# Kernel optimization log

Measured on AMD Instinct MI355X. Metric: run time of the kernel, lower is better.

## Reference

```python
import jax, jax.numpy as jnp
import numpy as np

B, C = 32768, 1000
EPS = 1e-6

def setup_inputs() -> dict:
    key = jax.random.key(0)
    k1, k2 = jax.random.split(key)
    # p_tar / p_vlm are probability distributions over C classes
    p_tar = jax.nn.softmax(jax.random.normal(k1, (B, C), dtype=jnp.float32), axis=1)
    p_vlm = jax.nn.softmax(jax.random.normal(k2, (B, C), dtype=jnp.float32), axis=1)
    alpha = jnp.array([0.99], dtype=jnp.float32)  # EMA momentum
    memory_bank = jnp.full((C, C), 1.0 / C, dtype=jnp.float32)  # __init__ state
    return {"p_tar": p_tar, "p_vlm": p_vlm, "alpha": alpha, "memory_bank": memory_bank}

def _uncertainty(p):
    return -p * jnp.log(p + EPS)

def reference(p_tar, p_vlm, alpha, memory_bank):
    n_classes = memory_bank.shape[0]
    norm = 1.0 / jnp.sqrt(jnp.float32(n_classes))
    # --- class_prototype_atten (uses PRE-update memory bank, as in torch) ---
    atten = jax.nn.softmax(jnp.matmul(p_tar, memory_bank.T) * norm, axis=1)  # [B, C]
    p_tar_new = jnp.matmul(atten, memory_bank)  # [B, C]
    # --- update_membank: vectorized per-class masked-mean EMA ---
    y_tar = jnp.argmax(p_tar, axis=1)
    y_vlm = jnp.argmax(p_vlm, axis=1)
    agree = y_tar == y_vlm
    # non-agreeing rows dumped into extra segment n_classes
    seg = jnp.where(agree, y_tar, n_classes)
    sums = jax.ops.segment_sum(p_tar, seg, num_segments=n_classes + 1)[:n_classes]  # [C, C]
    counts = jax.ops.segment_sum(agree.astype(p_tar.dtype), seg, num_segments=n_classes + 1)[:n_classes]  # [C]
    has = counts > 0
    mean = sums / jnp.where(has, counts, 1.0)[:, None]
    a = alpha.reshape(())
    bank_new = jnp.where(has[:, None], a * memory_bank + (1.0 - a) * mean, memory_bank)
    # --- uncertainty_mixing ---
    eu_tar = jnp.exp(-_uncertainty(p_tar_new))
    eu_vlm = jnp.exp(-_uncertainty(p_vlm))
    p_mix = (eu_tar * p_tar_new + eu_vlm * p_vlm) / (eu_tar + eu_vlm)
    return p_mix, bank_new
```

## Files before the change

### kernel.cpp

```cpp
#include <hip/hip_runtime.h>
#include <hip/hip_bf16.h>
#include <cstdint>
#include <cstddef>

#define NROWS 32768
#define NCLS  1000
#define KP    1024
#define NCH   32

typedef unsigned short u16;
typedef __bf16 bf16x8 __attribute__((ext_vector_type(8)));
typedef float  f32x4  __attribute__((ext_vector_type(4)));


__device__ __forceinline__ void gld_lds16(const u16* g, u16* l) {
  __builtin_amdgcn_global_load_lds(
      (const __attribute__((address_space(1))) unsigned int*)g,
      (__attribute__((address_space(3))) unsigned int*)l, 16, 0, 0);
}

__global__ __launch_bounds__(128)
void prep4_bank(const float* __restrict__ bank,
                __hip_bfloat16* __restrict__ M4,
                __hip_bfloat16* __restrict__ MT4) {
  __shared__ float tile[32][33];
  const int tx = blockIdx.x;
  const int ty = blockIdx.y;
  const int t  = threadIdx.x;
  {
    const int r = t >> 2, c0 = (t & 3) * 8;
    const int gj = ty * 32 + r;
    #pragma unroll
    for (int j = 0; j < 8; ++j) {
      const int gk = tx * 32 + c0 + j;
      tile[r][c0 + j] = (gj < NCLS && gk < NCLS) ? bank[gj * NCLS + gk] : 0.0f;
    }
  }
  __syncthreads();
  const int w = t >> 6, lane = t & 63, lr = lane & 15, qq = lane >> 4;
  if (w == 0) {
    #pragma unroll
    for (int s = 0; s < 2; ++s) {
      bf16x8 o;
      #pragma unroll
      for (int j = 0; j < 8; ++j) o[j] = (__bf16)tile[s * 16 + lr][qq * 8 + j];
      *(bf16x8*)((u16*)M4 + ((size_t)(ty * 2 + s) * NCH + tx) * 512 + lane * 8) = o;
    }
  } else {
    #pragma unroll
    for (int s = 0; s < 2; ++s) {
      bf16x8 o;
      #pragma unroll
      for (int j = 0; j < 8; ++j) o[j] = (__bf16)tile[qq * 8 + j][s * 16 + lr];
      *(bf16x8*)((u16*)MT4 + ((size_t)(tx * 2 + s) * NCH + ty) * 512 + lane * 8) = o;
    }
  }
}

__global__ __launch_bounds__(256)
void rows4_kernel(const float* __restrict__ p_tar, const float* __restrict__ p_vlm,
                  __hip_bfloat16* __restrict__ A4,
                  float* __restrict__ sums, float* __restrict__ counts) {
  const int w = threadIdx.x >> 6, lane = threadIdx.x & 63;
  const int lr = lane & 15, q = lane >> 4;
  const int panel = blockIdx.x * 4 + w;
  const int row   = panel * 16 + lr;
  const float* tr = p_tar + (size_t)row * NCLS;
  const float* vr = p_vlm + (size_t)row * NCLS;
  u16* a4 = (u16*)A4 + (size_t)panel * NCH * 512 + lane * 8;

  float bvT = -1.0f; int biT = 0;
  float bvV = -1.0f; int biV = 0;
  for (int c = 0; c < NCH; ++c) {
    const int k0 = c * 32 + q * 8;
    float v[8];
    if (k0 < NCLS) {
      float4 x = *(const float4*)(tr + k0);
      float4 y = *(const float4*)(tr + k0 + 4);
      v[0] = x.x; v[1] = x.y; v[2] = x.z; v[3] = x.w;
      v[4] = y.x; v[5] = y.y; v[6] = y.z; v[7] = y.w;
    } else {
      #pragma unroll
      for (int j = 0; j < 8; ++j) v[j] = 0.0f;
    }
    bf16x8 o;
    #pragma unroll
    for (int j = 0; j < 8; ++j) {
      o[j] = (__bf16)v[j];
      if (v[j] > bvT) { bvT = v[j]; biT = k0 + j; }
    }
    *(bf16x8*)(a4 + (size_t)c * 512) = o;
    if (k0 < NCLS) {
      float4 x = *(const float4*)(vr + k0);
      float4 y = *(const float4*)(vr + k0 + 4);
      float u[8] = {x.x, x.y, x.z, x.w, y.x, y.y, y.z, y.w};
      #pragma unroll
      for (int j = 0; j < 8; ++j)
        if (u[j] > bvV) { bvV = u[j]; biV = k0 + j; }
    }
  }
  #pragma unroll
  for (int d = 16; d < 64; d <<= 1) {
    float ov = __shfl_xor(bvT, d); int oi = __shfl_xor(biT, d);
    if (ov > bvT || (ov == bvT && oi < biT)) { bvT = ov; biT = oi; }
    float ov2 = __shfl_xor(bvV, d); int oi2 = __shfl_xor(biV, d);
    if (ov2 > bvV || (ov2 == bvV && oi2 < biV)) { bvV = ov2; biV = oi2; }
  }
  const int ag = (biT == biV) ? 1 : 0;
  for (int rr = 0; rr < 16; ++rr) {
    const int agr = __shfl(ag, rr);
    if (agr) {
      const int cls = __shfl(biT, rr);
      const float* trr = p_tar + (size_t)(panel * 16 + rr) * NCLS;
      for (int k = lane; k < NCLS; k += 64)
        atomicAdd(&sums[(size_t)cls * NCLS + k], trr[k]);
      if (lane == 0) atomicAdd(&counts[cls], 1.0f);
    }
  }
}

template <int WHICH>
__global__ __launch_bounds__(256, 4)
void gemm4(const u16* __restrict__ A4, const u16* __restrict__ B4,
           __hip_bfloat16* __restrict__ E4out, float* __restrict__ rowsum,
           const float* __restrict__ p_vlm, float* __restrict__ mix_out) {
  __shared__ u16 SH[4][4096];
  const int tid  = threadIdx.x;
  const int w    = tid >> 6;
  const int lane = tid & 63;
  const int lr   = lane & 15;
  const int q    = lane >> 4;
  const int L    = blockIdx.x;
  const int xcd  = L & 7;
  const int jj   = L >> 3;
  const int bm   = xcd * 32 + (jj >> 3);
  const int bn   = jj & 7;
  const int wm   = w >> 1;
  const int wn   = w & 1;

  f32x4 acc[4][4] = {};

  const u16* ga0 = A4 + ((size_t)(bm * 8 + 2 * w) * NCH) * 512 + lane * 8;
  const u16* ga1 = ga0 + (size_t)NCH * 512;
  const u16* gb0 = B4 + ((size_t)(bn * 8 + 2 * w) * NCH) * 512 + lane * 8;
  const u16* gb1 = gb0 + (size_t)NCH * 512;

  gld_lds16(ga0, &SH[0][(2 * w + 0) * 512]);
  gld_lds16(ga1, &SH[0][(2 * w + 1) * 512]);
  gld_lds16(gb0, &SH[2][(2 * w + 0) * 512]);
  gld_lds16(gb1, &SH[2][(2 * w + 1) * 512]);

  for (int i = 0; i < NCH; ++i) {
    const int cur = i & 1;
    __syncthreads();
    if (i + 1 < NCH) {
      const int nxt = cur ^ 1;
      const size_t ko = (size_t)(i + 1) * 512;
      gld_lds16(ga0 + ko, &SH[nxt][(2 * w + 0) * 512]);
      gld_lds16(ga1 + ko, &SH[nxt][(2 * w + 1) * 512]);
      gld_lds16(gb0 + ko, &SH[2 + nxt][(2 * w + 0) * 512]);
      gld_lds16(gb1 + ko, &SH[2 + nxt][(2 * w + 1) * 512]);
    }
    bf16x8 af[4], bfr[4];
    #pragma unroll
    for (int t = 0; t < 4; ++t) {
      af[t]  = *(const bf16x8*)(&SH[cur][(wm * 4 + t) * 512 + lane * 8]);
      bfr[t] = *(const bf16x8*)(&SH[2 + cur][(wn * 4 + t) * 512 + lane * 8]);
    }
    #pragma unroll
    for (int mt = 0; mt < 4; ++mt)
      #pragma unroll
      for (int nt = 0; nt < 4; ++nt)
        acc[mt][nt] = __builtin_amdgcn_mfma_f32_16x16x32_bf16(af[mt], bfr[nt], acc[mt][nt], 0, 0, 0);
  }

  const float NORM = 0.03162277660168379f;
  if (WHICH == 1) {
    __syncthreads();
    u16* ep = &SH[w][0];
    #pragma unroll
    for (int mt = 0; mt < 4; ++mt) {
      float psum[4] = {0.f, 0.f, 0.f, 0.f};
      #pragma unroll
      for (int nt = 0; nt < 4; ++nt) {
        const int gn = bn * 128 + wn * 64 + nt * 16 + lr;
        const int cc = nt >> 1;
        const int q2 = (nt & 1) * 2 + (lr >> 3);
        const int jj2 = lr & 7;
        #pragma unroll
        for (int r = 0; r < 4; ++r) {
          float e = (gn < NCLS) ? __expf(acc[mt][nt][r] * NORM) : 0.0f;
          psum[r] += e;
          __hip_bfloat16 h = __float2bfloat16(e);
          ep[(mt * 2 + cc) * 512 + (q2 * 16 + q * 4 + r) * 8 + jj2] = *(u16*)&h;
        }
      }
      #pragma unroll
      for (int r = 0; r < 4; ++r) {
        float s = psum[r];
        s += __shfl_xor(s, 1); s += __shfl_xor(s, 2);
        s += __shfl_xor(s, 4); s += __shfl_xor(s, 8);
        if (lr == 0) atomicAdd(&rowsum[bm * 128 + wm * 64 + mt * 16 + q * 4 + r], s);
      }
    }
    #pragma unroll
    for (int ch = 0; ch < 8; ++ch) {
      const int mt = ch >> 1, cc = ch & 1;
      bf16x8 v = *(const bf16x8*)(&ep[ch * 512 + lane * 8]);
      const size_t Rg = bm * 8 + wm * 4 + mt;
      const size_t cg = bn * 4 + wn * 2 + cc;
      *(bf16x8*)((u16*)E4out + (Rg * NCH + cg) * 512 + lane * 8) = v;
    }
  } else {
    #pragma unroll
    for (int mt = 0; mt < 4; ++mt) {
      #pragma unroll
      for (int r = 0; r < 4; ++r) {
        const int gm = bm * 128 + wm * 64 + mt * 16 + q * 4 + r;
        const float inv = 1.0f / rowsum[gm];
        #pragma unroll
        for (int nt = 0; nt < 4; ++nt) {
          const int gn = bn * 128 + wn * 64 + nt * 16 + lr;
          if (gn < NCLS) {
            float pt = acc[mt][nt][r] * inv;
            float pv = p_vlm[(size_t)gm * NCLS + gn];
            float et = __expf(pt * __logf(pt + 1e-6f));
            float ev = __expf(pv * __logf(pv + 1e-6f));
            mix_out[(size_t)gm * NCLS + gn] = (et * pt + ev * pv) / (et + ev);
          }
        }
      }
    }
  }
}

__global__ __launch_bounds__(256)
void bank_update(const float* __restrict__ bank, const float* __restrict__ sums,
                 const float* __restrict__ counts, const float* __restrict__ alpha,
                 float* __restrict__ out) {
  const int idx = blockIdx.x * 256 + threadIdx.x;
  if (idx >= NCLS * NCLS) return;
  const int r = idx / NCLS;
  const float cnt = counts[r];
  const float bv  = bank[idx];
  const float a   = alpha[0];
  out[idx] = (cnt > 0.0f) ? a * bv + (1.0f - a) * (sums[idx] / cnt) : bv;
}

extern "C" void kernel_launch(void* const* d_in, const int* in_sizes, int n_in,
                              void* d_out, int out_size, void* d_ws, size_t ws_size,
                              hipStream_t stream) {
  const float* p_tar = (const float*)d_in[0];
  const float* p_vlm = (const float*)d_in[1];
  const float* alpha = (const float*)d_in[2];
  const float* bank  = (const float*)d_in[3];
  float* out_mix  = (float*)d_out;
  float* out_bank = (float*)d_out + (size_t)NROWS * NCLS;

  char* w = (char*)d_ws;
  __hip_bfloat16* A4  = (__hip_bfloat16*)w; w += (size_t)NROWS * KP * 2;
  __hip_bfloat16* E4  = (__hip_bfloat16*)w; w += (size_t)NROWS * KP * 2;
  __hip_bfloat16* M4  = (__hip_bfloat16*)w; w += (size_t)KP * KP * 2;
  __hip_bfloat16* MT4 = (__hip_bfloat16*)w; w += (size_t)KP * KP * 2;
  float* sums   = (float*)w;                w += (size_t)NCLS * NCLS * 4;
  float* counts = (float*)w;                w += 1024 * 4;
  float* rs     = (float*)w;                w += (size_t)NROWS * 4;

  hipMemsetAsync(sums, 0, (size_t)NCLS * NCLS * 4 + 1024 * 4 + (size_t)NROWS * 4, stream);

  prep4_bank<<<dim3(32, 32), 128, 0, stream>>>(bank, M4, MT4);
  rows4_kernel<<<NROWS / 64, 256, 0, stream>>>(p_tar, p_vlm, A4, sums, counts);
  gemm4<1><<<2048, 256, 0, stream>>>(
      (const u16*)A4, (const u16*)M4, E4, rs, nullptr, nullptr);
  gemm4<2><<<2048, 256, 0, stream>>>(
      (const u16*)E4, (const u16*)MT4, nullptr, rs, p_vlm, out_mix);
  bank_update<<<(NCLS * NCLS + 255) / 256, 256, 0, stream>>>(bank, sums, counts, alpha, out_bank);
}
```

Before: 549.2 us.

## Triple-buffer GEMM LDS pipeline, split row-prep across waves, simplify mixing math

The GEMM main loop moves from a double-buffered LDS pipeline to a three-stage one, using explicit vmcnt waits and a raw barrier so two K-chunks are in flight. This costs more LDS and lowers the occupancy hint from 4 to 3 blocks. The row-prep kernel now has each block own one 16-row panel, with the four waves splitting the K range and merging argmax results through shared memory; this gives more blocks and shorter per-thread loops, but only one wave issues the atomics. The mixing epilogue is rewritten algebraically to use one exp of a difference instead of two exps.

```diff
diff --git a/kernel.cpp b/kernel.cpp
--- a/kernel.cpp
+++ b/kernel.cpp
@@ -61,9 +61,11 @@
 void rows4_kernel(const float* __restrict__ p_tar, const float* __restrict__ p_vlm,
                   __hip_bfloat16* __restrict__ A4,
                   float* __restrict__ sums, float* __restrict__ counts) {
+  __shared__ float sT[4][16]; __shared__ int siT[4][16];
+  __shared__ float sV[4][16]; __shared__ int siV[4][16];
   const int w = threadIdx.x >> 6, lane = threadIdx.x & 63;
   const int lr = lane & 15, q = lane >> 4;
-  const int panel = blockIdx.x * 4 + w;
+  const int panel = blockIdx.x;
   const int row   = panel * 16 + lr;
   const float* tr = p_tar + (size_t)row * NCLS;
   const float* vr = p_vlm + (size_t)row * NCLS;
@@ -71,7 +73,7 @@
 
   float bvT = -1.0f; int biT = 0;
   float bvV = -1.0f; int biV = 0;
-  for (int c = 0; c < NCH; ++c) {
+  for (int c = w * 8; c < w * 8 + 8; ++c) {
     const int k0 = c * 32 + q * 8;
     float v[8];
     if (k0 < NCLS) {
@@ -106,25 +108,36 @@
     float ov2 = __shfl_xor(bvV, d); int oi2 = __shfl_xor(biV, d);
     if (ov2 > bvV || (ov2 == bvV && oi2 < biV)) { bvV = ov2; biV = oi2; }
   }
-  const int ag = (biT == biV) ? 1 : 0;
-  for (int rr = 0; rr < 16; ++rr) {
-    const int agr = __shfl(ag, rr);
-    if (agr) {
-      const int cls = __shfl(biT, rr);
-      const float* trr = p_tar + (size_t)(panel * 16 + rr) * NCLS;
-      for (int k = lane; k < NCLS; k += 64)
-        atomicAdd(&sums[(size_t)cls * NCLS + k], trr[k]);
-      if (lane == 0) atomicAdd(&counts[cls], 1.0f);
+  if (q == 0) { sT[w][lr] = bvT; siT[w][lr] = biT; sV[w][lr] = bvV; siV[w][lr] = biV; }
+  __syncthreads();
+  float cT = sT[0][lr]; int ciT = siT[0][lr];
+  float cV = sV[0][lr]; int ciV = siV[0][lr];
+  #pragma unroll
+  for (int ww = 1; ww < 4; ++ww) {
+    float v1 = sT[ww][lr]; if (v1 > cT) { cT = v1; ciT = siT[ww][lr]; }
+    float v2 = sV[ww][lr]; if (v2 > cV) { cV = v2; ciV = siV[ww][lr]; }
+  }
+  if (w == 0) {
+    const int ag = (ciT == ciV) ? 1 : 0;
+    for (int rr = 0; rr < 16; ++rr) {
+      const int agr = __shfl(ag, rr);
+      if (agr) {
+        const int cls = __shfl(ciT, rr);
+        const float* trr = p_tar + (size_t)(panel * 16 + rr) * NCLS;
+        for (int k = lane; k < NCLS; k += 64)
+          atomicAdd(&sums[(size_t)cls * NCLS + k], trr[k]);
+        if (lane == 0) atomicAdd(&counts[cls], 1.0f);
+      }
     }
   }
 }
 
 template <int WHICH>
-__global__ __launch_bounds__(256, 4)
+__global__ __launch_bounds__(256, 3)
 void gemm4(const u16* __restrict__ A4, const u16* __restrict__ B4,
            __hip_bfloat16* __restrict__ E4out, float* __restrict__ rowsum,
            const float* __restrict__ p_vlm, float* __restrict__ mix_out) {
-  __shared__ u16 SH[4][4096];
+  __shared__ u16 SH[6][4096];
   const int tid  = threadIdx.x;
   const int w    = tid >> 6;
   const int lane = tid & 63;
@@ -145,34 +158,45 @@
   const u16* gb0 = B4 + ((size_t)(bn * 8 + 2 * w) * NCH) * 512 + lane * 8;
   const u16* gb1 = gb0 + (size_t)NCH * 512;
 
-  gld_lds16(ga0, &SH[0][(2 * w + 0) * 512]);
-  gld_lds16(ga1, &SH[0][(2 * w + 1) * 512]);
-  gld_lds16(gb0, &SH[2][(2 * w + 0) * 512]);
-  gld_lds16(gb1, &SH[2][(2 * w + 1) * 512]);
-
+  #define STAGE4(kk, b)                                            \
+    do {                                                           \
+      const size_t ko = (size_t)(kk) * 512;                        \
+      gld_lds16(ga0 + ko, &SH[(b)][(2 * w + 0) * 512]);            \
+      gld_lds16(ga1 + ko, &SH[(b)][(2 * w + 1) * 512]);            \
+      gld_lds16(gb0 + ko, &SH[3 + (b)][(2 * w + 0) * 512]);        \
+      gld_lds16(gb1 + ko, &SH[3 + (b)][(2 * w + 1) * 512]);        \
+    } while (0)
+
+  STAGE4(0, 0);
+  STAGE4(1, 1);
+
+  int cur = 0;
   for (int i = 0; i < NCH; ++i) {
-    const int cur = i & 1;
-    __syncthreads();
-    if (i + 1 < NCH) {
-      const int nxt = cur ^ 1;
-      const size_t ko = (size_t)(i + 1) * 512;
-      gld_lds16(ga0 + ko, &SH[nxt][(2 * w + 0) * 512]);
-      gld_lds16(ga1 + ko, &SH[nxt][(2 * w + 1) * 512]);
-      gld_lds16(gb0 + ko, &SH[2 + nxt][(2 * w + 0) * 512]);
-      gld_lds16(gb1 + ko, &SH[2 + nxt][(2 * w + 1) * 512]);
+    if (i < NCH - 1) {
+      asm volatile("s_waitcnt vmcnt(4)" ::: "memory");
+    } else {
+      asm volatile("s_waitcnt vmcnt(0)" ::: "memory");
+    }
+    __builtin_amdgcn_s_barrier();
+    asm volatile("" ::: "memory");
+    if (i + 2 < NCH) {
+      int b2 = cur + 2; if (b2 >= 3) b2 -= 3;
+      STAGE4(i + 2, b2);
     }
     bf16x8 af[4], bfr[4];
     #pragma unroll
     for (int t = 0; t < 4; ++t) {
       af[t]  = *(const bf16x8*)(&SH[cur][(wm * 4 + t) * 512 + lane * 8]);
-      bfr[t] = *(const bf16x8*)(&SH[2 + cur][(wn * 4 + t) * 512 + lane * 8]);
+      bfr[t] = *(const bf16x8*)(&SH[3 + cur][(wn * 4 + t) * 512 + lane * 8]);
     }
     #pragma unroll
     for (int mt = 0; mt < 4; ++mt)
       #pragma unroll
       for (int nt = 0; nt < 4; ++nt)
         acc[mt][nt] = __builtin_amdgcn_mfma_f32_16x16x32_bf16(af[mt], bfr[nt], acc[mt][nt], 0, 0, 0);
-  }
+    cur = (cur == 2) ? 0 : cur + 1;
+  }
+  #undef STAGE4
 
   const float NORM = 0.03162277660168379f;
   if (WHICH == 1) {
@@ -224,9 +248,10 @@
           if (gn < NCLS) {
             float pt = acc[mt][nt][r] * inv;
             float pv = p_vlm[(size_t)gm * NCLS + gn];
-            float et = __expf(pt * __logf(pt + 1e-6f));
-            float ev = __expf(pv * __logf(pv + 1e-6f));
-            mix_out[(size_t)gm * NCLS + gn] = (et * pt + ev * pv) / (et + ev);
+            float lt = pt * __logf(pt + 1e-6f);
+            float lv = pv * __logf(pv + 1e-6f);
+            float rr = __expf(lv - lt);
+            mix_out[(size_t)gm * NCLS + gn] = (pt + rr * pv) / (1.0f + rr);
           }
         }
       }
@@ -269,7 +294,7 @@
   hipMemsetAsync(sums, 0, (size_t)NCLS * NCLS * 4 + 1024 * 4 + (size_t)NROWS * 4, stream);
 
   prep4_bank<<<dim3(32, 32), 128, 0, stream>>>(bank, M4, MT4);
-  rows4_kernel<<<NROWS / 64, 256, 0, stream>>>(p_tar, p_vlm, A4, sums, counts);
+  rows4_kernel<<<NROWS / 16, 256, 0, stream>>>(p_tar, p_vlm, A4, sums, counts);
   gemm4<1><<<2048, 256, 0, stream>>>(
       (const u16*)A4, (const u16*)M4, E4, rs, nullptr, nullptr);
   gemm4<2><<<2048, 256, 0, stream>>>(
```

Result: slower. 565.2 us (+2.9%).
